# Performance work log

Measured on AMD Instinct MI355X. Metric: run time of the kernel, lower is better.

Reference implementation:

```python
import jax, jax.numpy as jnp
import numpy as np

N = 100_000       # nodes
E = 1_600_000     # edges
G = 128           # graphs in batch
RAW_ND, RAW_ED = 9, 3
ND, ED, H = 16, 2, 32  # node_dim, edge_dim, GAT hidden (heads=1)


def _p(key, shape, scale=0.1):
    return jax.random.normal(key, shape, dtype=jnp.float32) * scale


def setup_inputs() -> dict:
    key = jax.random.key(0)
    ks = jax.random.split(key, 32)
    inp = {
        "node_feat": jax.random.normal(ks[0], (N, RAW_ND), dtype=jnp.float32),
        "edge_index": jax.random.randint(ks[1], (2, E), 0, N, dtype=jnp.int64)
        if jax.config.jax_enable_x64 else jax.random.randint(ks[1], (2, E), 0, N).astype(jnp.int32),
        "edge_attr": jax.random.normal(ks[2], (E, RAW_ED), dtype=jnp.float32),
        "batch": jnp.sort(jax.random.randint(ks[3], (N,), 0, G)).astype(jnp.int32),
        # encoders
        "W_ne": _p(ks[4], (RAW_ND, ND)), "b_ne": jnp.zeros((ND,), jnp.float32),
        "W_ee": _p(ks[5], (RAW_ED, ED)), "b_ee": jnp.zeros((ED,), jnp.float32),
        # readout
        "W_l3": _p(ks[6], (3 * H, 1)), "b_l3": jnp.zeros((1,), jnp.float32),
    }
    dims_in = [ND, H, H]
    for i in range(3):
        k = jax.random.split(ks[7 + i], 6)
        inp[f"W{i}"] = _p(k[0], (dims_in[i], H))
        inp[f"as{i}"] = _p(k[1], (H,))
        inp[f"ad{i}"] = _p(k[2], (H,))
        inp[f"We{i}"] = _p(k[3], (ED, H))
        inp[f"ae{i}"] = _p(k[4], (H,))
        inp[f"bb{i}"] = jnp.zeros((H,), jnp.float32)
    return inp


def _segment_softmax(logits, seg, num_segments):
    m = jax.ops.segment_max(logits, seg, num_segments=num_segments)
    m = jnp.where(jnp.isfinite(m), m, 0.0)
    e = jnp.exp(logits - m[seg])
    s = jax.ops.segment_sum(e, seg, num_segments=num_segments)
    return e / (s[seg] + 1e-16)


def _gat(x, src, dst, ef, W, a_s, a_d, We, a_e, b):
    # PyG GATConv, heads=1, negative_slope=0.2
    h = x @ W                                   # [N', H]
    a_src = h @ a_s                             # [N']
    a_dst = h @ a_d
    a_edge = (ef @ We) @ a_e                    # [E']
    logits = jax.nn.leaky_relu(a_src[src] + a_dst[dst] + a_edge, 0.2)
    att = _segment_softmax(logits, dst, h.shape[0])
    out = jax.ops.segment_sum(h[src] * att[:, None], dst, num_segments=h.shape[0])
    return out + b


def reference(node_feat, edge_index, edge_attr, batch,
              W_ne, b_ne, W_ee, b_ee, W_l3, b_l3,
              W0, as0, ad0, We0, ae0, bb0,
              W1, as1, ad1, We1, ae1, bb1,
              W2, as2, ad2, We2, ae2, bb2):
    n = node_feat.shape[0]
    x = node_feat @ W_ne + b_ne                 # NodeEncoder -> [N,16]
    ef = edge_attr @ W_ee + b_ee                # EdgeEncoder -> [E,2]
    # add_self_loops=True with fill_value='mean' (PyG default when edge_dim set)
    loop = jnp.arange(n, dtype=edge_index.dtype)
    src = jnp.concatenate([edge_index[0], loop])
    dst = jnp.concatenate([edge_index[1], loop])
    ef_fill = jnp.broadcast_to(ef.mean(axis=0), (n, ef.shape[1]))
    ef_aug = jnp.concatenate([ef, ef_fill], axis=0)
    x1 = _gat(x, src, dst, ef_aug, W0, as0, ad0, We0, ae0, bb0)
    x2 = _gat(x1, src, dst, ef_aug, W1, as1, ad1, We1, ae1, bb1)
    x3 = _gat(x2, src, dst, ef_aug, W2, as2, ad2, We2, ae2, bb2)
    x_cat = jnp.concatenate([x1, x2, x3], axis=1)  # [N, 96]
    sums = jax.ops.segment_sum(x_cat, batch, num_segments=G)
    cnt = jax.ops.segment_sum(jnp.ones((n,), x_cat.dtype), batch, num_segments=G)
    pooled = sums / jnp.maximum(cnt, 1.0)[:, None]   # global mean pool [G,96]
    return pooled @ W_l3 + b_l3                      # [G,1]
```

## Files before the change

### kernel.cpp

```cpp
#include <hip/hip_runtime.h>
#include <hip/hip_fp16.h>


#define NBUCK_SHIFT 8
#define NBUCK_MAX 512
#define CAP 6144

__global__ void k_pre(const float4* __restrict__ ea4, const float* __restrict__ Wee,
                      const float* __restrict__ bee, float2* __restrict__ partial,
                      const int* __restrict__ ei1, int* __restrict__ bucket_cnt,
                      const int* __restrict__ batch, int* __restrict__ bounds,
                      const float* __restrict__ Wne, const float* __restrict__ bne,
                      const float* __restrict__ W0, float* __restrict__ wf,
                      int n, int e, int ep, int nbCS, int nbH) {
    int b = blockIdx.x, t = threadIdx.x;
    if (b < nbCS) {
        int tid = b * 256 + t;
        int e4 = e >> 2;
        float s0 = 0.f, s1 = 0.f;
        if (tid < e4) {
            float4 q0 = ea4[tid * 3], q1 = ea4[tid * 3 + 1], q2 = ea4[tid * 3 + 2];
            float a = q0.x + q0.w + q1.z + q2.y;
            float b2 = q0.y + q1.x + q1.w + q2.z;
            float c = q0.z + q1.y + q2.x + q2.w;
            s0 = a * Wee[0] + b2 * Wee[2] + c * Wee[4] + 4.f * bee[0];
            s1 = a * Wee[1] + b2 * Wee[3] + c * Wee[5] + 4.f * bee[1];
        }
#pragma unroll
        for (int off = 32; off > 0; off >>= 1) {
            s0 += __shfl_xor(s0, off, 64);
            s1 += __shfl_xor(s1, off, 64);
        }
        if ((t & 63) == 0)
            partial[(b << 2) + (t >> 6)] = make_float2(s0, s1);
        return;
    }
    b -= nbCS;
    if (b < nbH) {
        __shared__ int lh[NBUCK_MAX];
        lh[t] = 0; lh[t + 256] = 0;
        __syncthreads();
        int base = b * 4096;
#pragma unroll
        for (int i = 0; i < 16; ++i) {
            int gid = base + i * 256 + t;
            if (gid < ep) {
                int d = (gid < e) ? ei1[gid] : gid - e;
                atomicAdd(&lh[d >> NBUCK_SHIFT], 1);
            }
        }
        __syncthreads();
        if (lh[t]) atomicAdd(&bucket_cnt[t], lh[t]);
        if (lh[t + 256]) atomicAdd(&bucket_cnt[t + 256], lh[t + 256]);
        return;
    }
    for (int i = t; i < 288; i += 256) {
        int m = i >> 5, j = i & 31;
        float a = 0.f;
        for (int k = 0; k < 16; ++k) a += Wne[m * 16 + k] * W0[k * 32 + j];
        wf[i] = a;
    }
    if (t < 32) {
        float a = 0.f;
        for (int k = 0; k < 16; ++k) a += bne[k] * W0[k * 32 + t];
        wf[288 + t] = a;
    }
    for (int g = t; g <= 128; g += 256) {
        if (g == 128) { bounds[128] = n; continue; }
        int lo = 0, hi = n;
        while (lo < hi) {
            int mid = (lo + hi) >> 1;
            if (batch[mid] < g) lo = mid + 1; else hi = mid;
        }
        bounds[g] = lo;
    }
}

__global__ void k_hproj0(const float* __restrict__ nf, const float* __restrict__ wf,
                         const float* __restrict__ as_, const float* __restrict__ ad_,
                         unsigned int* __restrict__ h2, float* __restrict__ asrc,
                         float* __restrict__ adst, int n) {
    int node = blockIdx.x * 8 + (threadIdx.x >> 5);
    int j = threadIdx.x & 31;
    if (node >= n) return;
    const float* xr = nf + node * 9;
    float acc = wf[288 + j];
#pragma unroll
    for (int m = 0; m < 9; ++m) acc += xr[m] * wf[m * 32 + j];
    float accp = __shfl_down(acc, 1, 32);
    if ((j & 1) == 0) {
        __half2 hh = __floats2half2_rn(acc, accp);
        h2[(size_t)node * 16 + (j >> 1)] = *reinterpret_cast<unsigned int*>(&hh);
    }
    float r1 = acc * as_[j], r2 = acc * ad_[j];
#pragma unroll
    for (int off = 16; off > 0; off >>= 1) {
        r1 += __shfl_xor(r1, off, 32);
        r2 += __shfl_xor(r2, off, 32);
    }
    if (j == 0) { asrc[node] = r1; adst[node] = r2; }
}

__global__ void __launch_bounds__(512)
k_mid(const float* __restrict__ We0, const float* __restrict__ ae0,
      const float* __restrict__ We1, const float* __restrict__ ae1,
      const float* __restrict__ We2, const float* __restrict__ ae2,
      const float2* __restrict__ partial, int nw, float einv,
      float* __restrict__ consts,
      const int* __restrict__ bucket_cnt, int* __restrict__ bucket_base,
      int* __restrict__ bcursor, int nbuck, int ep, int* __restrict__ rp, int n) {
    int t = threadIdx.x;
    if (blockIdx.x == 0) {
        __shared__ float r0[512], r1[512];
        float m0 = 0.f, m1 = 0.f;
        for (int i = t; i < nw; i += 512) {
            float2 v = partial[i];
            m0 += v.x; m1 += v.y;
        }
        r0[t] = m0; r1[t] = m1;
        __syncthreads();
        for (int o = 256; o > 0; o >>= 1) {
            if (t < o) { r0[t] += r0[t + o]; r1[t] += r1[t + o]; }
            __syncthreads();
        }
        if (t == 0) {
            consts[12] = r0[0] * einv;
            consts[13] = r1[0] * einv;
            const float* We[3] = {We0, We1, We2};
            const float* ae[3] = {ae0, ae1, ae2};
            for (int l = 0; l < 3; ++l) {
                float c0 = 0.f, c1 = 0.f;
                for (int j = 0; j < 32; ++j) {
                    c0 += We[l][j] * ae[l][j];
                    c1 += We[l][32 + j] * ae[l][j];
                }
                consts[l * 2 + 0] = c0;
                consts[l * 2 + 1] = c1;
            }
        }
    } else {
        __shared__ int s[512];
        int v = (t < nbuck) ? bucket_cnt[t] : 0;
        s[t] = v;
        __syncthreads();
        for (int o = 1; o < 512; o <<= 1) {
            int x = (t >= o) ? s[t - o] : 0;
            __syncthreads();
            s[t] += x;
            __syncthreads();
        }
        int ex = s[t] - v;
        if (t < nbuck) { bucket_base[t] = ex; bcursor[t] = ex; }
        if (t == 0) { bucket_base[nbuck] = ep; rp[n] = ep; }
    }
}

__global__ void k_binB(const int* __restrict__ ei0, const int* __restrict__ ei1,
                       const float* __restrict__ ea, const float* __restrict__ We,
                       const float* __restrict__ be, const float* __restrict__ consts,
                       int* __restrict__ bcursor, uint2* __restrict__ st, int e, int ep) {
    __shared__ int lh[NBUCK_MAX], lcur[NBUCK_MAX];
    int t = threadIdx.x;
    lh[t] = 0; lh[t + 256] = 0;
    __syncthreads();
    int base = blockIdx.x * 4096;
    unsigned int sd[16], fh[16];
    int bk[16];
    float w00 = We[0], w10 = We[2], w20 = We[4];
    float w01 = We[1], w11 = We[3], w21 = We[5];
    float b0 = be[0], b1 = be[1];
#pragma unroll
    for (int i = 0; i < 16; ++i) {
        int gid = base + i * 256 + t;
        bk[i] = -1;
        if (gid < ep) {
            int s, d; float f0, f1;
            if (gid < e) {
                s = ei0[gid]; d = ei1[gid];
                const float* r = ea + (size_t)gid * 3;
                float a0 = r[0], a1 = r[1], a2 = r[2];
                f0 = a0 * w00 + a1 * w10 + a2 * w20 + b0;
                f1 = a0 * w01 + a1 * w11 + a2 * w21 + b1;
            } else {
                s = d = gid - e;
                f0 = consts[12]; f1 = consts[13];
            }
            bk[i] = d >> NBUCK_SHIFT;
            sd[i] = ((unsigned int)s << NBUCK_SHIFT) | (unsigned int)(d & 255);
            __half2 hh = __floats2half2_rn(f0, f1);
            fh[i] = *reinterpret_cast<unsigned int*>(&hh);
            atomicAdd(&lh[bk[i]], 1);
        }
    }
    __syncthreads();
    if (lh[t] > 0) lcur[t] = atomicAdd(&bcursor[t], lh[t]);
    if (lh[t + 256] > 0) lcur[t + 256] = atomicAdd(&bcursor[t + 256], lh[t + 256]);
    __syncthreads();
#pragma unroll
    for (int i = 0; i < 16; ++i) {
        if (bk[i] >= 0) {
            int pos = atomicAdd(&lcur[bk[i]], 1);
            st[pos] = make_uint2(sd[i], fh[i]);
        }
    }
}

__global__ void __launch_bounds__(512)
k_binC(const uint2* __restrict__ st, const int* __restrict__ bucket_base,
       int* __restrict__ rp, uint2* __restrict__ rec, int n) {
    __shared__ int nh[256], ns[256];
    __shared__ uint2 rs[CAP];
    int k = blockIdx.x, t = threadIdx.x;
    int s0 = bucket_base[k], s1 = bucket_base[k + 1];
    int cnt = s1 - s0;
    if (t < 256) nh[t] = 0;
    __syncthreads();
    for (int i = s0 + t; i < s1; i += 512)
        atomicAdd(&nh[st[i].x & 255], 1);
    __syncthreads();
    if (t < 256) ns[t] = nh[t];
    __syncthreads();
    for (int o = 1; o < 256; o <<= 1) {
        int add = 0;
        if (t < 256 && t >= o) add = ns[t - o];
        __syncthreads();
        if (t < 256) ns[t] += add;
        __syncthreads();
    }
    int node0 = k << NBUCK_SHIFT;
    if (t < 256) {
        int startl = ns[t] - nh[t];
        if (node0 + t < n) rp[node0 + t] = s0 + startl;
        nh[t] = startl;
    }
    __syncthreads();
    for (int i = s0 + t; i < s1; i += 512) {
        uint2 v = st[i];
        int pos = atomicAdd(&nh[v.x & 255], 1);
        uint2 r = make_uint2(v.x >> NBUCK_SHIFT, v.y);
        if (pos < CAP) rs[pos] = r;
        else rec[s0 + pos] = r;
    }
    __syncthreads();
    int m = cnt < CAP ? cnt : CAP;
    for (int i = t; i < m; i += 512)
        rec[s0 + i] = rs[i];
}

__device__ __forceinline__ float h2_get(const unsigned int* __restrict__ h2,
                                        int s, int word, bool hi) {
    unsigned int hw = h2[(size_t)s * 16 + word];
    __half2 hh = *reinterpret_cast<__half2*>(&hw);
    return hi ? __high2float(hh) : __low2float(hh);
}

template <bool HAS_NEXT>
__global__ void k_agg(const int* __restrict__ rp, const uint2* __restrict__ rec,
                      const float* __restrict__ asrcIn, const float* __restrict__ adstIn,
                      const float* __restrict__ consts, const unsigned int* __restrict__ h2in,
                      const float* __restrict__ bb, const float* __restrict__ Wn,
                      const float* __restrict__ asn, const float* __restrict__ adn_,
                      unsigned int* __restrict__ h2out, float* __restrict__ asrcOut,
                      float* __restrict__ adstOut, const float* __restrict__ wl3,
                      float* __restrict__ vout, int n, int layer) {
    __shared__ float sW[1024];
    if (HAS_NEXT) {
        for (int i = threadIdx.x; i < 1024; i += 256) sW[i] = Wn[i];
        __syncthreads();
    }
    int node = blockIdx.x * 8 + (threadIdx.x >> 5);
    int j = threadIdx.x & 31;
    if (node >= n) return;
    float c0 = consts[layer * 2], c1 = consts[layer * 2 + 1];
    int r0 = rp[node], r1 = rp[node + 1];
    float adn = adstIn[node];
    int word = j >> 1;
    bool hi = (j & 1) != 0;
    float acc = 0.f, psum = 0.f;
    for (int c = r0; c < r1; c += 32) {
        int i = c + j;
        float pe = 0.f; int s = 0;
        if (i < r1) {
            unsigned long long rv = __builtin_nontemporal_load(
                reinterpret_cast<const unsigned long long*>(rec + i));
            s = (int)(unsigned int)(rv & 0xffffffffull);
            unsigned int fv = (unsigned int)(rv >> 32);
            __half2 hh = *reinterpret_cast<__half2*>(&fv);
            float lg = asrcIn[s] + adn + __low2float(hh) * c0 + __high2float(hh) * c1;
            lg = lg > 0.f ? lg : 0.2f * lg;
            pe = __expf(lg);
        }
        psum += pe;
        int cnt = min(32, r1 - c);
        int t = 0;
        for (; t + 8 <= cnt; t += 8) {
            int s0 = __shfl(s, t, 32),     s1 = __shfl(s, t + 1, 32);
            int s2 = __shfl(s, t + 2, 32), s3 = __shfl(s, t + 3, 32);
            int s4 = __shfl(s, t + 4, 32), s5 = __shfl(s, t + 5, 32);
            int s6 = __shfl(s, t + 6, 32), s7 = __shfl(s, t + 7, 32);
            float p0 = __shfl(pe, t, 32),     p1 = __shfl(pe, t + 1, 32);
            float p2 = __shfl(pe, t + 2, 32), p3 = __shfl(pe, t + 3, 32);
            float p4 = __shfl(pe, t + 4, 32), p5 = __shfl(pe, t + 5, 32);
            float p6 = __shfl(pe, t + 6, 32), p7 = __shfl(pe, t + 7, 32);
            float h0 = h2_get(h2in, s0, word, hi);
            float h1 = h2_get(h2in, s1, word, hi);
            float h2v = h2_get(h2in, s2, word, hi);
            float h3 = h2_get(h2in, s3, word, hi);
            float h4 = h2_get(h2in, s4, word, hi);
            float h5 = h2_get(h2in, s5, word, hi);
            float h6 = h2_get(h2in, s6, word, hi);
            float h7 = h2_get(h2in, s7, word, hi);
            acc += p0 * h0; acc += p1 * h1; acc += p2 * h2v; acc += p3 * h3;
            acc += p4 * h4; acc += p5 * h5; acc += p6 * h6; acc += p7 * h7;
        }
        for (; t + 4 <= cnt; t += 4) {
            int s0 = __shfl(s, t, 32),     s1 = __shfl(s, t + 1, 32);
            int s2 = __shfl(s, t + 2, 32), s3 = __shfl(s, t + 3, 32);
            float p0 = __shfl(pe, t, 32),     p1 = __shfl(pe, t + 1, 32);
            float p2 = __shfl(pe, t + 2, 32), p3 = __shfl(pe, t + 3, 32);
            float h0 = h2_get(h2in, s0, word, hi);
            float h1 = h2_get(h2in, s1, word, hi);
            float h2v = h2_get(h2in, s2, word, hi);
            float h3 = h2_get(h2in, s3, word, hi);
            acc += p0 * h0; acc += p1 * h1; acc += p2 * h2v; acc += p3 * h3;
        }
        for (; t < cnt; ++t) {
            int st2 = __shfl(s, t, 32);
            float pt = __shfl(pe, t, 32);
            acc += pt * h2_get(h2in, st2, word, hi);
        }
    }
#pragma unroll
    for (int off = 16; off > 0; off >>= 1) psum += __shfl_xor(psum, off, 32);
    float res = acc / (psum + 1e-16f) + bb[j];
    float v = res * wl3[j];
#pragma unroll
    for (int off = 16; off > 0; off >>= 1) v += __shfl_xor(v, off, 32);
    if (j == 0) vout[node] = v;
    if (HAS_NEXT) {
        float hn = 0.f;
#pragma unroll
        for (int k = 0; k < 32; ++k)
            hn += __shfl(res, k, 32) * sW[k * 32 + j];
        float hnp = __shfl_down(hn, 1, 32);
        if ((j & 1) == 0) {
            __half2 hh = __floats2half2_rn(hn, hnp);
            h2out[(size_t)node * 16 + (j >> 1)] = *reinterpret_cast<unsigned int*>(&hh);
        }
        float r1n = hn * asn[j], r2n = hn * adn_[j];
#pragma unroll
        for (int off = 16; off > 0; off >>= 1) {
            r1n += __shfl_xor(r1n, off, 32);
            r2n += __shfl_xor(r2n, off, 32);
        }
        if (j == 0) { asrcOut[node] = r1n; adstOut[node] = r2n; }
    }
}

__global__ void k_dotv(const float* __restrict__ v0, const float* __restrict__ v1,
                       const float* __restrict__ v2, const int* __restrict__ bounds,
                       const float* __restrict__ bl3, float* __restrict__ out) {
    __shared__ float red[256];
    int g = blockIdx.x, t = threadIdx.x;
    int s0 = bounds[g], s1 = bounds[g + 1];
    float acc = 0.f;
    for (int i = s0 + t; i < s1; i += 256) acc += v0[i] + v1[i] + v2[i];
    red[t] = acc;
    __syncthreads();
    for (int o = 128; o > 0; o >>= 1) {
        if (t < o) red[t] += red[t + o];
        __syncthreads();
    }
    if (t == 0) {
        float c = (float)(s1 - s0);
        if (c < 1.f) c = 1.f;
        out[g] = red[0] / c + bl3[0];
    }
}

extern "C" void kernel_launch(void* const* d_in, const int* in_sizes, int n_in,
                              void* d_out, int out_size, void* d_ws, size_t ws_size,
                              hipStream_t stream) {
    (void)n_in; (void)out_size; (void)ws_size;
    const float* nf    = (const float*)d_in[0];
    const int*   ei    = (const int*)d_in[1];
    const float* ea    = (const float*)d_in[2];
    const int*   batch = (const int*)d_in[3];
    const float* W_ne  = (const float*)d_in[4];
    const float* b_ne  = (const float*)d_in[5];
    const float* W_ee  = (const float*)d_in[6];
    const float* b_ee  = (const float*)d_in[7];
    const float* W_l3  = (const float*)d_in[8];
    const float* b_l3  = (const float*)d_in[9];
    const float *Wl[3], *asl[3], *adl[3], *Wel[3], *ael[3], *bbl[3];
    for (int l = 0; l < 3; ++l) {
        Wl[l]  = (const float*)d_in[10 + 6 * l];
        asl[l] = (const float*)d_in[11 + 6 * l];
        adl[l] = (const float*)d_in[12 + 6 * l];
        Wel[l] = (const float*)d_in[13 + 6 * l];
        ael[l] = (const float*)d_in[14 + 6 * l];
        bbl[l] = (const float*)d_in[15 + 6 * l];
    }

    const int n  = in_sizes[3];
    const int e  = in_sizes[2] / 3;
    const int ep = e + n;
    const int* ei0 = ei;
    const int* ei1 = ei + e;
    const int nbuck = (n + 255) >> NBUCK_SHIFT;

    char* w = (char*)d_ws;
    size_t off = 0;
    auto alloc = [&](size_t b) { size_t o = off; off = (off + b + 255) & ~(size_t)255; return o; };
    unsigned int* h2a     = (unsigned int*)(w + alloc((size_t)n * 16 * 4));
    unsigned int* h2b     = (unsigned int*)(w + alloc((size_t)n * 16 * 4));
    float*        asrcA   = (float*)(w + alloc((size_t)n * 4));
    float*        adstA   = (float*)(w + alloc((size_t)n * 4));
    float*        asrcB   = (float*)(w + alloc((size_t)n * 4));
    float*        adstB   = (float*)(w + alloc((size_t)n * 4));
    float*        v0      = (float*)(w + alloc((size_t)n * 4));
    float*        v1      = (float*)(w + alloc((size_t)n * 4));
    float*        v2      = (float*)(w + alloc((size_t)n * 4));
    uint2*        st      = (uint2*)(w + alloc((size_t)ep * 8));
    uint2*        rec     = (uint2*)(w + alloc((size_t)ep * 8));
    int*          rp      = (int*)(w + alloc((size_t)(n + 1) * 4));
    int*          bcnt    = (int*)(w + alloc(NBUCK_MAX * 4));
    int*          bbase   = (int*)(w + alloc((NBUCK_MAX + 1) * 4));
    int*          bcur    = (int*)(w + alloc(NBUCK_MAX * 4));
    float2*       partial = (float2*)(w + alloc((size_t)8192 * 8));
    float*        consts  = (float*)(w + alloc(256));
    int*          bounds  = (int*)(w + alloc(129 * 4));
    float*        wfbuf   = (float*)(w + alloc(320 * 4));

    hipMemsetAsync(bcnt, 0, NBUCK_MAX * 4, stream);

    int e4   = e >> 2;
    int nbCS = (e4 + 255) / 256;
    int nbH  = (ep + 4095) / 4096;
    int nw   = nbCS * 4;
    int nbN  = (n + 7) / 8;

    k_pre<<<nbCS + nbH + 1, 256, 0, stream>>>(
        (const float4*)ea, W_ee, b_ee, partial, ei1, bcnt, batch, bounds,
        W_ne, b_ne, Wl[0], wfbuf, n, e, ep, nbCS, nbH);
    k_hproj0<<<nbN, 256, 0, stream>>>(nf, wfbuf, asl[0], adl[0],
                                      h2a, asrcA, adstA, n);
    k_mid<<<2, 512, 0, stream>>>(Wel[0], ael[0], Wel[1], ael[1], Wel[2], ael[2],
                                 partial, nw, 1.0f / (float)e, consts,
                                 bcnt, bbase, bcur, nbuck, ep, rp, n);
    k_binB<<<nbH, 256, 0, stream>>>(ei0, ei1, ea, W_ee, b_ee, consts, bcur, st, e, ep);
    k_binC<<<nbuck, 512, 0, stream>>>(st, bbase, rp, rec, n);

    k_agg<true><<<nbN, 256, 0, stream>>>(rp, rec, asrcA, adstA, consts, h2a,
                                         bbl[0], Wl[1], asl[1], adl[1],
                                         h2b, asrcB, adstB, W_l3 + 0, v0, n, 0);
    k_agg<true><<<nbN, 256, 0, stream>>>(rp, rec, asrcB, adstB, consts, h2b,
                                         bbl[1], Wl[2], asl[2], adl[2],
                                         h2a, asrcA, adstA, W_l3 + 32, v1, n, 1);
    k_agg<false><<<nbN, 256, 0, stream>>>(rp, rec, asrcA, adstA, consts, h2a,
                                          bbl[2], nullptr, nullptr, nullptr,
                                          nullptr, nullptr, nullptr,
                                          W_l3 + 64, v2, n, 2);
    k_dotv<<<128, 256, 0, stream>>>(v0, v1, v2, bounds, b_l3, (float*)d_out);
}
```

Baseline: 362.0 us.

## Split next-layer projection out of aggregation kernel; register-cache binning loads

```diff
diff --git a/kernel.cpp b/kernel.cpp
--- a/kernel.cpp
+++ b/kernel.cpp
@@ -87,6 +87,34 @@
     float acc = wf[288 + j];
 #pragma unroll
     for (int m = 0; m < 9; ++m) acc += xr[m] * wf[m * 32 + j];
+    float accp = __shfl_down(acc, 1, 32);
+    if ((j & 1) == 0) {
+        __half2 hh = __floats2half2_rn(acc, accp);
+        h2[(size_t)node * 16 + (j >> 1)] = *reinterpret_cast<unsigned int*>(&hh);
+    }
+    float r1 = acc * as_[j], r2 = acc * ad_[j];
+#pragma unroll
+    for (int off = 16; off > 0; off >>= 1) {
+        r1 += __shfl_xor(r1, off, 32);
+        r2 += __shfl_xor(r2, off, 32);
+    }
+    if (j == 0) { asrc[node] = r1; adst[node] = r2; }
+}
+
+__global__ void k_hproj(const float* __restrict__ x, const float* __restrict__ W,
+                        const float* __restrict__ as_, const float* __restrict__ ad_,
+                        unsigned int* __restrict__ h2, float* __restrict__ asrc,
+                        float* __restrict__ adst, int n) {
+    __shared__ float sW[1024];
+    for (int i = threadIdx.x; i < 1024; i += 256) sW[i] = W[i];
+    __syncthreads();
+    int node = blockIdx.x * 8 + (threadIdx.x >> 5);
+    int j = threadIdx.x & 31;
+    if (node >= n) return;
+    const float* xr = x + (size_t)node * 32;
+    float acc = 0.f;
+#pragma unroll
+    for (int k = 0; k < 32; ++k) acc += xr[k] * sW[k * 32 + j];
     float accp = __shfl_down(acc, 1, 32);
     if ((j & 1) == 0) {
         __half2 hh = __floats2half2_rn(acc, accp);
@@ -213,10 +241,18 @@
     int k = blockIdx.x, t = threadIdx.x;
     int s0 = bucket_base[k], s1 = bucket_base[k + 1];
     int cnt = s1 - s0;
+    uint2 lv[12];
     if (t < 256) nh[t] = 0;
     __syncthreads();
-    for (int i = s0 + t; i < s1; i += 512)
-        atomicAdd(&nh[st[i].x & 255], 1);
+#pragma unroll
+    for (int u = 0; u < 12; ++u) {
+        int i = s0 + u * 512 + t;
+        if (i < s1) {
+            uint2 v = st[i];
+            lv[u] = v;
+            atomicAdd(&nh[v.x & 255], 1);
+        }
+    }
     __syncthreads();
     if (t < 256) ns[t] = nh[t];
     __syncthreads();
@@ -234,12 +270,16 @@
         nh[t] = startl;
     }
     __syncthreads();
-    for (int i = s0 + t; i < s1; i += 512) {
-        uint2 v = st[i];
-        int pos = atomicAdd(&nh[v.x & 255], 1);
-        uint2 r = make_uint2(v.x >> NBUCK_SHIFT, v.y);
-        if (pos < CAP) rs[pos] = r;
-        else rec[s0 + pos] = r;
+#pragma unroll
+    for (int u = 0; u < 12; ++u) {
+        int i = s0 + u * 512 + t;
+        if (i < s1) {
+            uint2 v = lv[u];
+            int pos = atomicAdd(&nh[v.x & 255], 1);
+            uint2 r = make_uint2(v.x >> NBUCK_SHIFT, v.y);
+            if (pos < CAP) rs[pos] = r;
+            else rec[s0 + pos] = r;
+        }
     }
     __syncthreads();
     int m = cnt < CAP ? cnt : CAP;
@@ -254,26 +294,19 @@
     return hi ? __high2float(hh) : __low2float(hh);
 }
 
-template <bool HAS_NEXT>
+template <bool STORE_X>
 __global__ void k_agg(const int* __restrict__ rp, const uint2* __restrict__ rec,
-                      const float* __restrict__ asrcIn, const float* __restrict__ adstIn,
-                      const float* __restrict__ consts, const unsigned int* __restrict__ h2in,
-                      const float* __restrict__ bb, const float* __restrict__ Wn,
-                      const float* __restrict__ asn, const float* __restrict__ adn_,
-                      unsigned int* __restrict__ h2out, float* __restrict__ asrcOut,
-                      float* __restrict__ adstOut, const float* __restrict__ wl3,
-                      float* __restrict__ vout, int n, int layer) {
-    __shared__ float sW[1024];
-    if (HAS_NEXT) {
-        for (int i = threadIdx.x; i < 1024; i += 256) sW[i] = Wn[i];
-        __syncthreads();
-    }
+                      const float* __restrict__ asrc, const float* __restrict__ adst,
+                      const float* __restrict__ consts, const unsigned int* __restrict__ h2,
+                      const float* __restrict__ bb, float* __restrict__ xout,
+                      const float* __restrict__ wl3, float* __restrict__ vout,
+                      int n, int layer) {
     int node = blockIdx.x * 8 + (threadIdx.x >> 5);
     int j = threadIdx.x & 31;
     if (node >= n) return;
     float c0 = consts[layer * 2], c1 = consts[layer * 2 + 1];
     int r0 = rp[node], r1 = rp[node + 1];
-    float adn = adstIn[node];
+    float adn = adst[node];
     int word = j >> 1;
     bool hi = (j & 1) != 0;
     float acc = 0.f, psum = 0.f;
@@ -286,7 +319,7 @@
             s = (int)(unsigned int)(rv & 0xffffffffull);
             unsigned int fv = (unsigned int)(rv >> 32);
             __half2 hh = *reinterpret_cast<__half2*>(&fv);
-            float lg = asrcIn[s] + adn + __low2float(hh) * c0 + __high2float(hh) * c1;
+            float lg = asrc[s] + adn + __low2float(hh) * c0 + __high2float(hh) * c1;
             lg = lg > 0.f ? lg : 0.2f * lg;
             pe = __expf(lg);
         }
@@ -302,14 +335,14 @@
             float p2 = __shfl(pe, t + 2, 32), p3 = __shfl(pe, t + 3, 32);
             float p4 = __shfl(pe, t + 4, 32), p5 = __shfl(pe, t + 5, 32);
             float p6 = __shfl(pe, t + 6, 32), p7 = __shfl(pe, t + 7, 32);
-            float h0 = h2_get(h2in, s0, word, hi);
-            float h1 = h2_get(h2in, s1, word, hi);
-            float h2v = h2_get(h2in, s2, word, hi);
-            float h3 = h2_get(h2in, s3, word, hi);
-            float h4 = h2_get(h2in, s4, word, hi);
-            float h5 = h2_get(h2in, s5, word, hi);
-            float h6 = h2_get(h2in, s6, word, hi);
-            float h7 = h2_get(h2in, s7, word, hi);
+            float h0 = h2_get(h2, s0, word, hi);
+            float h1 = h2_get(h2, s1, word, hi);
+            float h2v = h2_get(h2, s2, word, hi);
+            float h3 = h2_get(h2, s3, word, hi);
+            float h4 = h2_get(h2, s4, word, hi);
+            float h5 = h2_get(h2, s5, word, hi);
+            float h6 = h2_get(h2, s6, word, hi);
+            float h7 = h2_get(h2, s7, word, hi);
             acc += p0 * h0; acc += p1 * h1; acc += p2 * h2v; acc += p3 * h3;
             acc += p4 * h4; acc += p5 * h5; acc += p6 * h6; acc += p7 * h7;
         }
@@ -318,43 +351,26 @@
             int s2 = __shfl(s, t + 2, 32), s3 = __shfl(s, t + 3, 32);
             float p0 = __shfl(pe, t, 32),     p1 = __shfl(pe, t + 1, 32);
             float p2 = __shfl(pe, t + 2, 32), p3 = __shfl(pe, t + 3, 32);
-            float h0 = h2_get(h2in, s0, word, hi);
-            float h1 = h2_get(h2in, s1, word, hi);
-            float h2v = h2_get(h2in, s2, word, hi);
-            float h3 = h2_get(h2in, s3, word, hi);
+            float h0 = h2_get(h2, s0, word, hi);
+            float h1 = h2_get(h2, s1, word, hi);
+            float h2v = h2_get(h2, s2, word, hi);
+            float h3 = h2_get(h2, s3, word, hi);
             acc += p0 * h0; acc += p1 * h1; acc += p2 * h2v; acc += p3 * h3;
         }
         for (; t < cnt; ++t) {
             int st2 = __shfl(s, t, 32);
             float pt = __shfl(pe, t, 32);
-            acc += pt * h2_get(h2in, st2, word, hi);
+            acc += pt * h2_get(h2, st2, word, hi);
         }
     }
 #pragma unroll
     for (int off = 16; off > 0; off >>= 1) psum += __shfl_xor(psum, off, 32);
     float res = acc / (psum + 1e-16f) + bb[j];
+    if (STORE_X) xout[(size_t)node * 32 + j] = res;
     float v = res * wl3[j];
 #pragma unroll
     for (int off = 16; off > 0; off >>= 1) v += __shfl_xor(v, off, 32);
     if (j == 0) vout[node] = v;
-    if (HAS_NEXT) {
-        float hn = 0.f;
-#pragma unroll
-        for (int k = 0; k < 32; ++k)
-            hn += __shfl(res, k, 32) * sW[k * 32 + j];
-        float hnp = __shfl_down(hn, 1, 32);
-        if ((j & 1) == 0) {
-            __half2 hh = __floats2half2_rn(hn, hnp);
-            h2out[(size_t)node * 16 + (j >> 1)] = *reinterpret_cast<unsigned int*>(&hh);
-        }
-        float r1n = hn * asn[j], r2n = hn * adn_[j];
-#pragma unroll
-        for (int off = 16; off > 0; off >>= 1) {
-            r1n += __shfl_xor(r1n, off, 32);
-            r2n += __shfl_xor(r2n, off, 32);
-        }
-        if (j == 0) { asrcOut[node] = r1n; adstOut[node] = r2n; }
-    }
 }
 
 __global__ void k_dotv(const float* __restrict__ v0, const float* __restrict__ v1,
@@ -412,6 +428,8 @@
     char* w = (char*)d_ws;
     size_t off = 0;
     auto alloc = [&](size_t b) { size_t o = off; off = (off + b + 255) & ~(size_t)255; return o; };
+    float*        x1      = (float*)(w + alloc((size_t)n * 32 * 4));
+    float*        x2      = (float*)(w + alloc((size_t)n * 32 * 4));
     unsigned int* h2a     = (unsigned int*)(w + alloc((size_t)n * 16 * 4));
     unsigned int* h2b     = (unsigned int*)(w + alloc((size_t)n * 16 * 4));
     float*        asrcA   = (float*)(w + alloc((size_t)n * 4));
@@ -452,14 +470,12 @@
     k_binC<<<nbuck, 512, 0, stream>>>(st, bbase, rp, rec, n);
 
     k_agg<true><<<nbN, 256, 0, stream>>>(rp, rec, asrcA, adstA, consts, h2a,
-                                         bbl[0], Wl[1], asl[1], adl[1],
-                                         h2b, asrcB, adstB, W_l3 + 0, v0, n, 0);
+                                         bbl[0], x1, W_l3 + 0, v0, n, 0);
+    k_hproj<<<nbN, 256, 0, stream>>>(x1, Wl[1], asl[1], adl[1], h2b, asrcB, adstB, n);
     k_agg<true><<<nbN, 256, 0, stream>>>(rp, rec, asrcB, adstB, consts, h2b,
-                                         bbl[1], Wl[2], asl[2], adl[2],
-                                         h2a, asrcA, adstA, W_l3 + 32, v1, n, 1);
+                                         bbl[1], x2, W_l3 + 32, v1, n, 1);
+    k_hproj<<<nbN, 256, 0, stream>>>(x2, Wl[2], asl[2], adl[2], h2a, asrcA, adstA, n);
     k_agg<false><<<nbN, 256, 0, stream>>>(rp, rec, asrcA, adstA, consts, h2a,
-                                          bbl[2], nullptr, nullptr, nullptr,
-                                          nullptr, nullptr, nullptr,
-                                          W_l3 + 64, v2, n, 2);
+                                          bbl[2], nullptr, W_l3 + 64, v2, n, 2);
     k_dotv<<<128, 256, 0, stream>>>(v0, v1, v2, bounds, b_l3, (float*)d_out);
 }
```

Result: faster. 348.3 us (-3.8%).
